# Kernel optimization log

Measured on AMD Instinct MI355X. Metric: run time of the kernel, lower is better.

Reference implementation:

```python
import jax, jax.numpy as jnp
import numpy as np


def _silu(x):
    return x * jax.nn.sigmoid(x)


def _silu_backprop(dy, x):
    s = jax.nn.sigmoid(x)
    return dy * s * (1.0 + x * (1.0 - s))


def setup_inputs() -> dict:
    key = jax.random.key(0)
    B, L, Din, Dh, Dout, C = 8, 8192, 256, 512, 256, 1024
    ks = jax.random.split(key, 9)
    w0 = jax.random.normal(ks[0], (B, Dh, Din), jnp.float32) * (Din ** -0.5)
    w1 = jax.random.normal(ks[1], (B, Dout, Dh), jnp.float32) * (Dh ** -0.5)
    w2 = jax.random.normal(ks[2], (B, Dh, Din), jnp.float32) * (Din ** -0.5)
    q = jax.random.normal(ks[3], (B, L, Din), jnp.float32)
    k = jax.random.normal(ks[4], (B, L, Din), jnp.float32)
    v = jax.random.normal(ks[5], (B, L, Dout), jnp.float32)
    # per-token learning rates (softplus-ish positive, small)
    lr0 = jax.random.uniform(ks[6], (B, L, 1), jnp.float32) * 0.01
    lr1 = jax.random.uniform(ks[7], (B, L, 1), jnp.float32) * 0.01
    lr2 = jax.random.uniform(ks[8], (B, L, 1), jnp.float32) * 0.01
    return {"w0": w0, "w1": w1, "w2": w2, "q": q, "k": k, "v": v,
            "lr0": lr0, "lr1": lr1, "lr2": lr2, "chunk_size": C}


def _apply_swiglu(w0, w1, w2, qi):
    # f(q) = w1 @ (silu(w0 @ q) * (w2 @ q)); qi: [B, C, Din] -> [B, C, Dout]
    g = jnp.einsum('bcd,bhd->bch', qi, w0)
    h = jnp.einsum('bcd,bhd->bch', qi, w2)
    return jnp.einsum('bch,boh->bco', _silu(g) * h, w1)


def reference(w0, w1, w2, q, k, v, lr0, lr1, lr2, chunk_size):
    B, L, Din = q.shape
    Dout = v.shape[-1]
    C = int(chunk_size)
    n = L // C  # seq_len assumed multiple of chunk_size
    eps = 1e-5

    # per-row norms of initial fast weights (prenorm target norms)
    w0n = jnp.linalg.norm(w0, axis=2, keepdims=True)
    w1n = jnp.linalg.norm(w1, axis=2, keepdims=True)
    w2n = jnp.linalg.norm(w2, axis=2, keepdims=True)

    def chunks(x):
        return x.reshape(B, n, C, x.shape[-1]).transpose(1, 0, 2, 3)  # [n,B,C,d]

    qc, kc, vc = chunks(q), chunks(k), chunks(v)
    l0c, l1c, l2c = chunks(lr0), chunks(lr1), chunks(lr2)

    def step(carry, xs):
        w0c, w1c, w2c, w0m, w1m, w2m = carry
        qi, ki, vi, l0, l1, l2 = xs
        # apply current fast weights to this chunk's queries
        out = _apply_swiglu(w0c, w1c, w2c, qi)
        # fast-weight SwiGLU forward on keys
        g = jnp.einsum('bcd,bhd->bch', ki, w0c)          # gate_before_act^T
        hb = jnp.einsum('bcd,bhd->bch', ki, w2c)         # hidden_before_mul^T
        sg = _silu(g)
        hidden = sg * hb                                  # [B,C,Dh]
        # backprop of dot(f(k), v) through the SwiGLU
        dh = jnp.einsum('bco,boh->bch', vi, w1c)          # dhidden^T
        dhbm = dh * sg                                    # dhidden_before_mul^T
        dg = dh * hb                                      # dgate^T
        dgba = _silu_backprop(dg, g)                      # dgate_before_act^T
        dw1 = jnp.einsum('bco,bch->boh', vi, hidden * l1)
        dw0 = jnp.einsum('bch,bcd->bhd', dgba, ki * l0)
        dw2 = jnp.einsum('bch,bcd->bhd', dhbm, ki * l2)
        # prenorm update: accumulate into main weights, renormalize rows
        w0m = w0m + dw0
        w1m = w1m + dw1
        w2m = w2m + dw2
        w0c = w0m / (jnp.linalg.norm(w0m, axis=2, keepdims=True) + eps) * w0n
        w1c = w1m / (jnp.linalg.norm(w1m, axis=2, keepdims=True) + eps) * w1n
        w2c = w2m / (jnp.linalg.norm(w2m, axis=2, keepdims=True) + eps) * w2n
        return (w0c, w1c, w2c, w0m, w1m, w2m), out

    init = (w0, w1, w2, w0, w1, w2)
    carry, outs = jax.lax.scan(
        step, init,
        (qc[:-1], kc[:-1], vc[:-1], l0c[:-1], l1c[:-1], l2c[:-1]))
    # last chunk is apply-only (shifted block-causal)
    last = _apply_swiglu(carry[0], carry[1], carry[2], qc[-1])
    out = jnp.concatenate(
        [outs.transpose(1, 0, 2, 3).reshape(B, (n - 1) * C, Dout), last], axis=1)
    return out
```

## Files before the change

### kernel.cpp

```cpp
#include <hip/hip_runtime.h>
#include <cmath>

typedef unsigned short u16;
typedef __attribute__((ext_vector_type(8))) short short8;
typedef __attribute__((ext_vector_type(4))) float f32x4;

#define DEVINL __device__ __forceinline__

constexpr int NB   = 8;
constexpr int LSEQ = 8192;
constexpr int DIN  = 256;
constexpr int DH   = 512;
constexpr int DOUT = 256;
constexpr int CHK  = 1024;
constexpr int NCHK = LSEQ / CHK;

DEVINL void split2f(float v, u16& h, u16& l) {
  unsigned u = __builtin_bit_cast(unsigned, v);
  u16 hh = (u16)(u >> 16);
  float fh = __builtin_bit_cast(float, (unsigned)hh << 16);
  float r = v - fh;
  h = hh;
  l = (u16)(__builtin_bit_cast(unsigned, r) >> 16);
}
DEVINL void split3f(float v, u16& h, u16& m, u16& l) {
  unsigned u = __builtin_bit_cast(unsigned, v);
  u16 hh = (u16)(u >> 16);
  float fh = __builtin_bit_cast(float, (unsigned)hh << 16);
  float r1 = v - fh;
  u16 mm = (u16)(__builtin_bit_cast(unsigned, r1) >> 16);
  float fm = __builtin_bit_cast(float, (unsigned)mm << 16);
  float r2 = r1 - fm;
  h = hh; m = mm;
  l = (u16)(__builtin_bit_cast(unsigned, r2) >> 16);
}

DEVINL void gl16(const u16* g, u16* l) {
  __builtin_amdgcn_global_load_lds(
      (const __attribute__((address_space(1))) unsigned int*)g,
      (__attribute__((address_space(3))) unsigned int*)l,
      16, 0, 0);
}

template<int BK> DEVINL int swz(int r) { return (BK == 64) ? (r & 7) : ((r >> 1) & 3); }

template<int BM, int BN, int BK, int NS, int DUAL, int EPI, int MERGE>
__global__ __launch_bounds__(256)
void k_gemm(const u16* A, const u16* D, const u16* B, const u16* E,
            long sLA, long sLB,
            float* __restrict__ out0, float* __restrict__ out1,
            u16* __restrict__ oh, u16* __restrict__ ol,
            int K, int ldo, long sAb, long sBb, long sOb,
            int NTX, int NTY,
            const u16* A2, const u16* B2, long sLA2, long sLB2,
            float* __restrict__ out2, int ldo2,
            long sA2b, long sB2b, long sO2b, int NTX2)
{
  constexpr int NA  = (DUAL == 1) ? 2 : 1;
  constexpr int NB_ = (DUAL == 2) ? 2 : 1;
  constexpr int NDUP = DUAL ? 2 : 1;
  constexpr int SLOTS = BK / 8;
  constexpr int RPC = 64 / SLOTS;
  constexpr int TBA = BM * BK;
  constexpr int TBB = BN * BK;
  constexpr int NTA = NA * NS, NTB = NB_ * NS;
  constexpr int CPA = BM / RPC, CPB = BN / RPC;
  constexpr int NCHUNK = NTA * CPA + NTB * CPB;
  constexpr int WM = BM / 2, WN = BN / 2, FM = WM / 16, FN = WN / 16;
  constexpr int NPROD = (NS == 2) ? 3 : 6;
  constexpr int KSTEPS = BK / 32;

  static constexpr int PSA[6] = {0, 0, 1, 0, 1, 2};
  static constexpr int PSB[6] = {0, 1, 0, 2, 1, 0};

  __shared__ alignas(16) u16 lds[(NTA * BM + NTB * BN) * BK];

  const int fid = blockIdx.x;
  const int b = fid & 7;
  int t = fid >> 3;
  int job = 0;
  if (MERGE) {
    if (t >= NTY * NTX) { job = 1; t -= NTY * NTX; }
  }
  const int ntx = (MERGE && job) ? NTX2 : NTX;
  const int my = t / ntx, nx = t % ntx;
  const int m0 = my * BM;
  const int n0 = nx * BN;

  const int tid = threadIdx.x, wid = tid >> 6, ln = tid & 63;
  const int wm = wid >> 1, wn = wid & 1;

  const u16* Ap; const u16* Dp = nullptr; const u16* Bp; const u16* Ep = nullptr;
  long eLA, eLB; int eldo; long eOb;
  if (MERGE && job) {
    Ap = A2 + (size_t)b * sA2b + (size_t)m0 * K;
    Bp = B2 + (size_t)b * sB2b + (size_t)n0 * K;
    eLA = sLA2; eLB = sLB2; eldo = ldo2; eOb = sO2b;
  } else {
    Ap = A + (size_t)b * sAb + (size_t)m0 * K;
    if (DUAL == 1) Dp = D + (size_t)b * sAb + (size_t)m0 * K;
    Bp = B + (size_t)b * sBb + (size_t)n0 * K;
    if (DUAL == 2) Ep = E + (size_t)b * sBb + (size_t)n0 * K;
    eLA = sLA; eLB = sLB; eldo = ldo; eOb = sOb;
  }

  f32x4 acc[NDUP][FM][FN];
#pragma unroll
  for (int d = 0; d < NDUP; ++d)
#pragma unroll
    for (int i = 0; i < FM; ++i)
#pragma unroll
      for (int j = 0; j < FN; ++j)
        acc[d][i][j] = (f32x4){0.f, 0.f, 0.f, 0.f};

  const int crow = ln / SLOTS;
  const int cslot = ln % SLOTS;

#pragma unroll 1
  for (int k0 = 0; k0 < K; k0 += BK) {
    for (int c = wid; c < NCHUNK; c += 4) {
      const u16* g;
      u16* ldst;
      if (c < NTA * CPA) {
        const int tile = c / CPA, rb = c % CPA;
        const int da = tile / NS, s = tile % NS;
        if (MERGE && job && da == 1) continue;
        const int r = rb * RPC + crow;
        const int kb = cslot ^ swz<BK>(r);
        const u16* base = (NA == 2 && da == 1) ? Dp : Ap;
        g = base + (size_t)s * eLA + (size_t)r * K + k0 + kb * 8;
        ldst = lds + tile * TBA + rb * (RPC * BK);
      } else {
        const int c2 = c - NTA * CPA;
        const int tile = c2 / CPB, rb = c2 % CPB;
        const int db = tile / NS, s = tile % NS;
        const int r = rb * RPC + crow;
        const int kb = cslot ^ swz<BK>(r);
        const u16* base = (NB_ == 2 && db == 1) ? Ep : Bp;
        g = base + (size_t)s * eLB + (size_t)r * K + k0 + kb * 8;
        ldst = lds + NTA * TBA + tile * TBB + rb * (RPC * BK);
      }
      gl16(g, ldst);
    }
    __syncthreads();

    const int ro = ln & 15, ko = ln >> 4;
#pragma unroll
    for (int ks = 0; ks < KSTEPS; ++ks) {
      short8 af[NA][NS][FM], bfr[NB_][NS][FN];
#pragma unroll
      for (int da = 0; da < NA; ++da) {
        if (MERGE && job && da == 1) continue;
#pragma unroll
        for (int s = 0; s < NS; ++s)
#pragma unroll
          for (int im = 0; im < FM; ++im) {
            const int row = wm * WM + im * 16 + ro;
            const int kb = ks * 4 + ko;
            const int phys = kb ^ swz<BK>(row);
            af[da][s][im] = *(const short8*)(lds + (da * NS + s) * TBA + row * BK + phys * 8);
          }
      }
#pragma unroll
      for (int db = 0; db < NB_; ++db)
#pragma unroll
        for (int s = 0; s < NS; ++s)
#pragma unroll
          for (int in = 0; in < FN; ++in) {
            const int row = wn * WN + in * 16 + ro;
            const int kb = ks * 4 + ko;
            const int phys = kb ^ swz<BK>(row);
            bfr[db][s][in] = *(const short8*)(lds + NTA * TBA + (db * NS + s) * TBB + row * BK + phys * 8);
          }
#pragma unroll
      for (int p = 0; p < NPROD; ++p) {
        const int sa = PSA[p], sb = PSB[p];
#pragma unroll
        for (int d = 0; d < NDUP; ++d) {
          if (MERGE && job && d == 1) continue;
          const int da = (DUAL == 1) ? d : 0;
          const int db = (DUAL == 2) ? d : 0;
#pragma unroll
          for (int im = 0; im < FM; ++im)
#pragma unroll
            for (int in = 0; in < FN; ++in)
              acc[d][im][in] = __builtin_amdgcn_mfma_f32_16x16x32_bf16(
                  af[da][sa][im], bfr[db][sb][in], acc[d][im][in], 0, 0, 0);
        }
      }
    }
    __syncthreads();
  }

#pragma unroll
  for (int im = 0; im < FM; ++im)
#pragma unroll
    for (int in = 0; in < FN; ++in)
#pragma unroll
      for (int r = 0; r < 4; ++r) {
        const int row = m0 + wm * WM + im * 16 + (ln >> 4) * 4 + r;
        const int col = n0 + wn * WN + in * 16 + (ln & 15);
        const size_t o = (size_t)b * eOb + (size_t)row * eldo + col;
        if (MERGE && job) {
          if (EPI == 1) out2[o] = acc[0][im][in][r];
          else          out2[o] += acc[0][im][in][r];
        } else if (EPI == 0) {
          out0[o] = acc[0][im][in][r];
        } else if (EPI == 1) {
          out0[o] = acc[0][im][in][r];
          out1[o] = acc[1][im][in][r];
        } else if (EPI == 2) {
          out0[o] += acc[0][im][in][r];
        } else if (EPI == 3) {
          out0[o] += acc[0][im][in][r];
          out1[o] += acc[1][im][in][r];
        } else {
          const float g = acc[0][im][in][r];
          const float h = acc[1][im][in][r];
          const float s = 1.f / (1.f + expf(-g));
          const float a = g * s * h;
          u16 hh, ll;
          split2f(a, hh, ll);
          oh[o] = hh;
          ol[o] = ll;
        }
      }
}

__global__ __launch_bounds__(256)
void k_bwd(const float* __restrict__ gT, const float* __restrict__ hT,
           const float* __restrict__ dT,
           const float* __restrict__ lr0, const float* __restrict__ lr1,
           const float* __restrict__ lr2,
           u16* __restrict__ gb0, u16* __restrict__ gb1, u16* __restrict__ gb2,
           u16* __restrict__ hb0, u16* __restrict__ hb1, u16* __restrict__ hb2,
           u16* __restrict__ hd0, u16* __restrict__ hd1, u16* __restrict__ hd2,
           int ch)
{
  const size_t i4 = (size_t)blockIdx.x * 256 + threadIdx.x;
  const size_t base = i4 * 4;
  const int c = (int)(base & 1023);
  const size_t bh = base >> 10;
  const int b = (int)(bh >> 9);
  const size_t li = (size_t)b * LSEQ + (size_t)ch * CHK + c;

  const float4 g4 = *(const float4*)&gT[base];
  const float4 h4 = *(const float4*)&hT[base];
  const float4 d4 = *(const float4*)&dT[base];
  const float4 L0 = *(const float4*)&lr0[li];
  const float4 L1 = *(const float4*)&lr1[li];
  const float4 L2 = *(const float4*)&lr2[li];
  const float gv[4] = {g4.x, g4.y, g4.z, g4.w};
  const float hv[4] = {h4.x, h4.y, h4.z, h4.w};
  const float dv[4] = {d4.x, d4.y, d4.z, d4.w};
  const float l0v[4] = {L0.x, L0.y, L0.z, L0.w};
  const float l1v[4] = {L1.x, L1.y, L1.z, L1.w};
  const float l2v[4] = {L2.x, L2.y, L2.z, L2.w};

  ushort4 og0, og1, og2, oh0, oh1, oh2, od0, od1, od2;
  u16* pg0 = &og0.x; u16* pg1 = &og1.x; u16* pg2 = &og2.x;
  u16* ph0 = &oh0.x; u16* ph1 = &oh1.x; u16* ph2 = &oh2.x;
  u16* pd0 = &od0.x; u16* pd1 = &od1.x; u16* pd2 = &od2.x;
#pragma unroll
  for (int t = 0; t < 4; ++t) {
    const float g = gv[t];
    const float sig = 1.f / (1.f + expf(-g));
    const float sg = g * sig;
    const float hidden = sg * hv[t];
    const float dhbm = dv[t] * sg;
    const float dgrad = dv[t] * hv[t];
    const float dgba = dgrad * sig * (1.f + g * (1.f - sig));
    split3f(dgba * l0v[t], pg0[t], pg1[t], pg2[t]);
    split3f(dhbm * l2v[t], ph0[t], ph1[t], ph2[t]);
    split3f(hidden * l1v[t], pd0[t], pd1[t], pd2[t]);
  }
  *(ushort4*)&gb0[base] = og0; *(ushort4*)&gb1[base] = og1; *(ushort4*)&gb2[base] = og2;
  *(ushort4*)&hb0[base] = oh0; *(ushort4*)&hb1[base] = oh1; *(ushort4*)&hb2[base] = oh2;
  *(ushort4*)&hd0[base] = od0; *(ushort4*)&hd1[base] = od1; *(ushort4*)&hd2[base] = od2;
}

__global__ __launch_bounds__(256)
void k_split3(const float* __restrict__ q, const float* __restrict__ k,
              const float* __restrict__ v,
              u16* __restrict__ q0, u16* __restrict__ q1,
              u16* __restrict__ k0s, u16* __restrict__ k1s, u16* __restrict__ k2s,
              u16* __restrict__ v0s, u16* __restrict__ v1s, u16* __restrict__ v2s,
              int ch)
{
  const int sec = blockIdx.y;
  const size_t base = ((size_t)blockIdx.x * 256 + threadIdx.x) * 4;
  const int b = (int)(base >> 18);
  const size_t rem = base & 0x3FFFF;
  const size_t soff = (size_t)b * (LSEQ * 256) + (size_t)ch * (CHK * 256) + rem;

  const float* src = (sec == 0) ? q : (sec == 1) ? k : v;
  const float4 x4 = *(const float4*)&src[soff];
  const float xv[4] = {x4.x, x4.y, x4.z, x4.w};

  if (sec == 0) {
    ushort4 a, bq;
    u16* pa = &a.x; u16* pb = &bq.x;
#pragma unroll
    for (int t = 0; t < 4; ++t) split2f(xv[t], pa[t], pb[t]);
    *(ushort4*)&q0[base] = a;
    *(ushort4*)&q1[base] = bq;
  } else {
    ushort4 a, bq, cq;
    u16* pa = &a.x; u16* pb = &bq.x; u16* pc = &cq.x;
#pragma unroll
    for (int t = 0; t < 4; ++t) split3f(xv[t], pa[t], pb[t], pc[t]);
    u16* d0 = (sec == 1) ? k0s : v0s;
    u16* d1 = (sec == 1) ? k1s : v1s;
    u16* d2 = (sec == 1) ? k2s : v2s;
    *(ushort4*)&d0[base] = a;
    *(ushort4*)&d1[base] = bq;
    *(ushort4*)&d2[base] = cq;
  }
}

__global__ __launch_bounds__(256)
void k_trans(const float* __restrict__ ksrc, const float* __restrict__ vsrc,
             u16* __restrict__ dk0, u16* __restrict__ dk1, u16* __restrict__ dk2,
             u16* __restrict__ dv0, u16* __restrict__ dv1, u16* __restrict__ dv2,
             int ch)
{
  __shared__ float T[64][65];
  const int b = blockIdx.z & 7;
  const int sel = blockIdx.z >> 3;
  const int ct = blockIdx.x;
  const int dt = blockIdx.y;
  const int tid = threadIdx.x;
  const float* src = sel ? vsrc : ksrc;
  u16* d0 = sel ? dv0 : dk0;
  u16* d1 = sel ? dv1 : dk1;
  u16* d2 = sel ? dv2 : dk2;
  const float* S = src + ((size_t)b * LSEQ + (size_t)ch * CHK + ct * 64) * 256 + dt * 64;

#pragma unroll
  for (int qq = 0; qq < 4; ++qq) {
    const int flat = qq * 256 + tid;
    const int r = flat >> 4;
    const int cq = (flat & 15) * 4;
    const float4 v4 = *(const float4*)&S[(size_t)r * 256 + cq];
    T[r][cq + 0] = v4.x; T[r][cq + 1] = v4.y; T[r][cq + 2] = v4.z; T[r][cq + 3] = v4.w;
  }
  __syncthreads();

  u16* D0 = d0 + (size_t)b * (256 * CHK) + (size_t)(dt * 64) * CHK + ct * 64;
  u16* D1 = d1 + (size_t)b * (256 * CHK) + (size_t)(dt * 64) * CHK + ct * 64;
  u16* D2 = d2 + (size_t)b * (256 * CHK) + (size_t)(dt * 64) * CHK + ct * 64;
#pragma unroll
  for (int qq = 0; qq < 4; ++qq) {
    const int flat = qq * 256 + tid;
    const int rr = flat >> 4;
    const int cc = (flat & 15) * 4;
    ushort4 a, bq, cq4;
    u16* pa = &a.x; u16* pb = &bq.x; u16* pc = &cq4.x;
#pragma unroll
    for (int i = 0; i < 4; ++i) split3f(T[cc + i][rr], pa[i], pb[i], pc[i]);
    const size_t o = (size_t)rr * CHK + cc;
    *(ushort4*)&D0[o] = a;
    *(ushort4*)&D1[o] = bq;
    *(ushort4*)&D2[o] = cq4;
  }
}

__global__ __launch_bounds__(256)
void k_w1t(const float* __restrict__ wm1, const float* __restrict__ scales,
           u16* __restrict__ d0, u16* __restrict__ d1, u16* __restrict__ d2)
{
  __shared__ float T[64][65];
  const int b = blockIdx.z;
  const int ot = blockIdx.x;
  const int ht = blockIdx.y;
  const int tid = threadIdx.x;
  const float* S = wm1 + (size_t)b * (256 * 512) + (size_t)(ot * 64) * 512 + ht * 64;
  const float* sc = scales + 4096 + b * 256 + ot * 64;

#pragma unroll
  for (int qq = 0; qq < 4; ++qq) {
    const int flat = qq * 256 + tid;
    const int r = flat >> 4;
    const int cq = (flat & 15) * 4;
    const float s = sc[r];
    const float4 v4 = *(const float4*)&S[(size_t)r * 512 + cq];
    T[r][cq + 0] = v4.x * s; T[r][cq + 1] = v4.y * s; T[r][cq + 2] = v4.z * s; T[r][cq + 3] = v4.w * s;
  }
  __syncthreads();

  u16* D0 = d0 + (size_t)b * (512 * 256) + (size_t)(ht * 64) * 256 + ot * 64;
  u16* D1 = d1 + (size_t)b * (512 * 256) + (size_t)(ht * 64) * 256 + ot * 64;
  u16* D2 = d2 + (size_t)b * (512 * 256) + (size_t)(ht * 64) * 256 + ot * 64;
#pragma unroll
  for (int qq = 0; qq < 4; ++qq) {
    const int flat = qq * 256 + tid;
    const int rr = flat >> 4;
    const int cc = (flat & 15) * 4;
    ushort4 a, bq, cq4;
    u16* pa = &a.x; u16* pb = &bq.x; u16* pc = &cq4.x;
#pragma unroll
    for (int i = 0; i < 4; ++i) split3f(T[cc + i][rr], pa[i], pb[i], pc[i]);
    const size_t o = (size_t)rr * 256 + cc;
    *(ushort4*)&D0[o] = a;
    *(ushort4*)&D1[o] = bq;
    *(ushort4*)&D2[o] = cq4;
  }
}

__global__ __launch_bounds__(256)
void k_wsplit(const float* __restrict__ wm0, const float* __restrict__ wm1,
              const float* __restrict__ wm2, const float* __restrict__ scales,
              u16* __restrict__ a00, u16* __restrict__ a01, u16* __restrict__ a02,
              u16* __restrict__ a10, u16* __restrict__ a11, u16* __restrict__ a12,
              u16* __restrict__ a20, u16* __restrict__ a21, u16* __restrict__ a22)
{
  const size_t e4 = ((size_t)blockIdx.x * 256 + threadIdx.x) * 4;
  const float* src; u16 *d0, *d1, *d2; float s; size_t off;
  if (e4 < 1048576) {
    off = e4; src = wm0; d0 = a00; d1 = a01; d2 = a02;
    s = scales[off >> 8];
  } else if (e4 < 2097152) {
    off = e4 - 1048576; src = wm1; d0 = a10; d1 = a11; d2 = a12;
    s = scales[4096 + (off >> 9)];
  } else {
    off = e4 - 2097152; src = wm2; d0 = a20; d1 = a21; d2 = a22;
    s = scales[6144 + (off >> 8)];
  }
  const float4 v4 = *(const float4*)&src[off];
  const float xv[4] = {v4.x * s, v4.y * s, v4.z * s, v4.w * s};
  ushort4 a, bq, cq;
  u16* pa = &a.x; u16* pb = &bq.x; u16* pc = &cq.x;
#pragma unroll
  for (int t = 0; t < 4; ++t) split3f(xv[t], pa[t], pb[t], pc[t]);
  *(ushort4*)&d0[off] = a;
  *(ushort4*)&d1[off] = bq;
  *(ushort4*)&d2[off] = cq;
}

__global__ __launch_bounds__(64)
void k_scalesplit(const float* __restrict__ wm0, const float* __restrict__ wm1,
                  const float* __restrict__ wm2, const float* __restrict__ wn,
                  float* __restrict__ scales,
                  u16* __restrict__ a00, u16* __restrict__ a01, u16* __restrict__ a02,
                  u16* __restrict__ a10, u16* __restrict__ a11, u16* __restrict__ a12,
                  u16* __restrict__ a20, u16* __restrict__ a21, u16* __restrict__ a22)
{
  const int row = blockIdx.x;
  const float* src; u16 *d0, *d1, *d2; int len; int r;
  if (row < 4096)      { r = row;        src = wm0; d0 = a00; d1 = a01; d2 = a02; len = 256; }
  else if (row < 6144) { r = row - 4096; src = wm1; d0 = a10; d1 = a11; d2 = a12; len = 512; }
  else                 { r = row - 6144; src = wm2; d0 = a20; d1 = a21; d2 = a22; len = 256; }
  const float* s = src + (size_t)r * len;
  float ss = 0.f;
  for (int i = threadIdx.x * 4; i < len; i += 256) {
    const float4 v4 = *(const float4*)&s[i];
    ss += v4.x * v4.x + v4.y * v4.y + v4.z * v4.z + v4.w * v4.w;
  }
#pragma unroll
  for (int off = 32; off > 0; off >>= 1) ss += __shfl_down(ss, off);
  ss = __shfl(ss, 0);
  const float scale = wn[row] / (sqrtf(ss) + 1e-5f);
  if (threadIdx.x == 0) scales[row] = scale;
  for (int i = threadIdx.x * 4; i < len; i += 256) {
    const float4 v4 = *(const float4*)&s[i];
    const float xv[4] = {v4.x * scale, v4.y * scale, v4.z * scale, v4.w * scale};
    ushort4 a, bq, cq;
    u16* pa = &a.x; u16* pb = &bq.x; u16* pc = &cq.x;
#pragma unroll
    for (int t = 0; t < 4; ++t) split3f(xv[t], pa[t], pb[t], pc[t]);
    const size_t o = (size_t)r * len + i;
    *(ushort4*)&d0[o] = a;
    *(ushort4*)&d1[o] = bq;
    *(ushort4*)&d2[o] = cq;
  }
}

__global__ __launch_bounds__(64)
void k_init(const float* __restrict__ w0, const float* __restrict__ w1,
            const float* __restrict__ w2,
            float* __restrict__ wm0, float* __restrict__ wm1, float* __restrict__ wm2,
            float* __restrict__ wn, float* __restrict__ scales)
{
  const int row = blockIdx.x;
  const float* src; float* dst; int len; int r;
  if (row < 4096)      { r = row;        src = w0; dst = wm0; len = 256; }
  else if (row < 6144) { r = row - 4096; src = w1; dst = wm1; len = 512; }
  else                 { r = row - 6144; src = w2; dst = wm2; len = 256; }
  const float* s = src + (size_t)r * len;
  float* d = dst + (size_t)r * len;
  float ss = 0.f;
  for (int i = threadIdx.x; i < len; i += 64) {
    const float v = s[i];
    d[i] = v;
    ss += v * v;
  }
#pragma unroll
  for (int off = 32; off > 0; off >>= 1) ss += __shfl_down(ss, off);
  if (threadIdx.x == 0) {
    wn[row] = sqrtf(ss);
    scales[row] = 1.f;
  }
}

extern "C" void kernel_launch(void* const* d_in, const int* in_sizes, int n_in,
                              void* d_out, int out_size, void* d_ws, size_t ws_size,
                              hipStream_t stream)
{
  const float* w0  = (const float*)d_in[0];
  const float* w1  = (const float*)d_in[1];
  const float* w2  = (const float*)d_in[2];
  const float* q   = (const float*)d_in[3];
  const float* k   = (const float*)d_in[4];
  const float* v   = (const float*)d_in[5];
  const float* lr0 = (const float*)d_in[6];
  const float* lr1 = (const float*)d_in[7];
  const float* lr2 = (const float*)d_in[8];
  float* out = (float*)d_out;

  float* p = (float*)d_ws;
  size_t o = 0;
  auto AF = [&](size_t n) { float* r = p + o; o += n; return r; };
  auto AH = [&](size_t n) { u16* r = (u16*)(p + o); o += n / 2; return r; };

  constexpr long WL = 1048576;
  constexpr long XL = 2097152;
  constexpr long HL = 4194304;

  float* wm0 = AF(1048576);
  float* wm1 = AF(1048576);
  float* wm2 = AF(1048576);
  float* wn = AF(10240);
  float* scales = AF(10240);
  float* gT  = AF(4194304);
  float* hT  = AF(4194304);
  float* dhT = AF(4194304);
  u16* w0s  = AH(3 * WL);
  u16* w2s  = AH(3 * WL);
  u16* w1s  = AH(3 * WL);
  u16* w1Ts = AH(3 * WL);
  u16* qs   = AH(2 * XL);
  u16* ks3  = AH(3 * XL);
  u16* vs3  = AH(3 * XL);
  u16* gbs  = AH(3 * HL);
  u16* hbs  = AH(3 * HL);
  u16* hds  = AH(3 * HL);
  u16* kTs  = ks3;
  u16* vTs  = vs3;
  u16* acts = gbs;

  k_init<<<10240, 64, 0, stream>>>(w0, w1, w2, wm0, wm1, wm2, wn, scales);
  k_wsplit<<<3072, 256, 0, stream>>>(wm0, wm1, wm2, scales,
      w0s, w0s + WL, w0s + 2 * WL, w1s, w1s + WL, w1s + 2 * WL,
      w2s, w2s + WL, w2s + 2 * WL);
  k_w1t<<<dim3(4, 8, NB), 256, 0, stream>>>(wm1, scales,
      w1Ts, w1Ts + WL, w1Ts + 2 * WL);

  for (int ch = 0; ch < NCHK; ++ch) {
    const bool last = (ch == NCHK - 1);
    k_split3<<<dim3(2048, last ? 1 : 3), 256, 0, stream>>>(q, k, v,
        qs, qs + XL, ks3, ks3 + XL, ks3 + 2 * XL, vs3, vs3 + XL, vs3 + 2 * XL, ch);

    k_gemm<128, 64, 64, 2, 2, 4, 0><<<512, 256, 0, stream>>>(
        qs, nullptr, w0s, w2s, XL, WL,
        nullptr, nullptr, acts, acts + HL,
        256, DH, 262144, 131072, (long)CHK * DH, 8, 8,
        nullptr, nullptr, 0, 0, nullptr, 0, 0, 0, 0, 0);
    k_gemm<128, 64, 64, 2, 0, 0, 0><<<256, 256, 0, stream>>>(
        acts, nullptr, w1s, nullptr, HL, WL,
        out + (size_t)ch * CHK * DOUT, nullptr, nullptr, nullptr,
        512, DOUT, (long)CHK * DH, 131072, (long)LSEQ * DOUT, 4, 8,
        nullptr, nullptr, 0, 0, nullptr, 0, 0, 0, 0, 0);

    if (last) break;

    k_gemm<64, 64, 32, 3, 1, 1, 1><<<2048, 256, 0, stream>>>(
        w0s, w2s, ks3, nullptr, WL, XL,
        gT, hT, nullptr, nullptr,
        256, CHK, 131072, 262144, (long)DH * CHK, 16, 8,
        w1Ts, vs3, WL, XL, dhT, CHK, 131072, 262144, (long)DH * CHK, 16);

    k_bwd<<<4096, 256, 0, stream>>>(gT, hT, dhT, lr0, lr1, lr2,
        gbs, gbs + HL, gbs + 2 * HL, hbs, hbs + HL, hbs + 2 * HL,
        hds, hds + HL, hds + 2 * HL, ch);

    k_trans<<<dim3(16, 4, 16), 256, 0, stream>>>(k, v,
        kTs, kTs + XL, kTs + 2 * XL, vTs, vTs + XL, vTs + 2 * XL, ch);

    k_gemm<64, 64, 32, 3, 1, 3, 1><<<512, 256, 0, stream>>>(
        gbs, hbs, kTs, nullptr, HL, XL,
        wm0, wm2, nullptr, nullptr,
        1024, DIN, (long)DH * CHK, (long)DIN * CHK, (long)DH * DIN, 4, 8,
        vTs, hds, XL, HL, wm1, DH, (long)DOUT * CHK, (long)DH * CHK,
        (long)DOUT * DH, 8);

    k_scalesplit<<<10240, 64, 0, stream>>>(wm0, wm1, wm2, wn, scales,
        w0s, w0s + WL, w0s + 2 * WL, w1s, w1s + WL, w1s + 2 * WL,
        w2s, w2s + WL, w2s + 2 * WL);
    k_w1t<<<dim3(4, 8, NB), 256, 0, stream>>>(wm1, scales,
        w1Ts, w1Ts + WL, w1Ts + 2 * WL);
  }
}
```

Baseline: 1.833 ms.

## Split-K the weight-gradient GEMM, enlarge backward tiles, reduce partials in scalesplit

The weight-gradient GEMM over the 1024-token chunk is split into four K-slices, each written as a partial into scratch buffers (gT/hT/dhT reused). The partials are summed into the main weights inside k_scalesplit, which then renormalizes and splits them. The forward-on-keys and dW GEMMs move from 64x64 to 128x128 tiles, and the fragment loads are restructured so B fragments are loaded per product pair, lowering register pressure. The intent is more data reuse per block and better parallelism for the long-K reduction. The cost is extra partial-buffer traffic and an extra read pass in scalesplit.

```diff
diff --git a/kernel.cpp b/kernel.cpp
--- a/kernel.cpp
+++ b/kernel.cpp
@@ -14,6 +14,8 @@
 constexpr int DOUT = 256;
 constexpr int CHK  = 1024;
 constexpr int NCHK = LSEQ / CHK;
+constexpr int DWSPLIT = 4;
+constexpr long PSTRIDE = 1048576;
 
 DEVINL void split2f(float v, u16& h, u16& l) {
   unsigned u = __builtin_bit_cast(unsigned, v);
@@ -44,13 +46,13 @@
 
 template<int BK> DEVINL int swz(int r) { return (BK == 64) ? (r & 7) : ((r >> 1) & 3); }
 
-template<int BM, int BN, int BK, int NS, int DUAL, int EPI, int MERGE>
+template<int BM, int BN, int BK, int NS, int DUAL, int EPI, int MERGE, int KSPLIT>
 __global__ __launch_bounds__(256)
 void k_gemm(const u16* A, const u16* D, const u16* B, const u16* E,
             long sLA, long sLB,
             float* __restrict__ out0, float* __restrict__ out1,
             u16* __restrict__ oh, u16* __restrict__ ol,
-            int K, int ldo, long sAb, long sBb, long sOb,
+            int K, int Klen, long sKp, int ldo, long sAb, long sBb, long sOb,
             int NTX, int NTY,
             const u16* A2, const u16* B2, long sLA2, long sLB2,
             float* __restrict__ out2, int ldo2,
@@ -67,11 +69,7 @@
   constexpr int CPA = BM / RPC, CPB = BN / RPC;
   constexpr int NCHUNK = NTA * CPA + NTB * CPB;
   constexpr int WM = BM / 2, WN = BN / 2, FM = WM / 16, FN = WN / 16;
-  constexpr int NPROD = (NS == 2) ? 3 : 6;
   constexpr int KSTEPS = BK / 32;
-
-  static constexpr int PSA[6] = {0, 0, 1, 0, 1, 2};
-  static constexpr int PSB[6] = {0, 1, 0, 2, 1, 0};
 
   __shared__ alignas(16) u16 lds[(NTA * BM + NTB * BN) * BK];
 
@@ -80,10 +78,12 @@
   int t = fid >> 3;
   int job = 0;
   if (MERGE) {
-    if (t >= NTY * NTX) { job = 1; t -= NTY * NTX; }
-  }
+    if (t >= NTY * NTX * KSPLIT) { job = 1; t -= NTY * NTX * KSPLIT; }
+  }
+  const int tile = t / KSPLIT;
+  const int ksid = t % KSPLIT;
   const int ntx = (MERGE && job) ? NTX2 : NTX;
-  const int my = t / ntx, nx = t % ntx;
+  const int my = tile / ntx, nx = tile % ntx;
   const int m0 = my * BM;
   const int n0 = nx * BN;
 
@@ -92,15 +92,16 @@
 
   const u16* Ap; const u16* Dp = nullptr; const u16* Bp; const u16* Ep = nullptr;
   long eLA, eLB; int eldo; long eOb;
+  const size_t kof = (size_t)ksid * Klen;
   if (MERGE && job) {
-    Ap = A2 + (size_t)b * sA2b + (size_t)m0 * K;
-    Bp = B2 + (size_t)b * sB2b + (size_t)n0 * K;
+    Ap = A2 + (size_t)b * sA2b + (size_t)m0 * K + kof;
+    Bp = B2 + (size_t)b * sB2b + (size_t)n0 * K + kof;
     eLA = sLA2; eLB = sLB2; eldo = ldo2; eOb = sO2b;
   } else {
-    Ap = A + (size_t)b * sAb + (size_t)m0 * K;
-    if (DUAL == 1) Dp = D + (size_t)b * sAb + (size_t)m0 * K;
-    Bp = B + (size_t)b * sBb + (size_t)n0 * K;
-    if (DUAL == 2) Ep = E + (size_t)b * sBb + (size_t)n0 * K;
+    Ap = A + (size_t)b * sAb + (size_t)m0 * K + kof;
+    if (DUAL == 1) Dp = D + (size_t)b * sAb + (size_t)m0 * K + kof;
+    Bp = B + (size_t)b * sBb + (size_t)n0 * K + kof;
+    if (DUAL == 2) Ep = E + (size_t)b * sBb + (size_t)n0 * K + kof;
     eLA = sLA; eLB = sLB; eldo = ldo; eOb = sOb;
   }
 
@@ -117,28 +118,28 @@
   const int cslot = ln % SLOTS;
 
 #pragma unroll 1
-  for (int k0 = 0; k0 < K; k0 += BK) {
+  for (int k0 = 0; k0 < Klen; k0 += BK) {
     for (int c = wid; c < NCHUNK; c += 4) {
       const u16* g;
       u16* ldst;
       if (c < NTA * CPA) {
-        const int tile = c / CPA, rb = c % CPA;
-        const int da = tile / NS, s = tile % NS;
+        const int tl = c / CPA, rb = c % CPA;
+        const int da = tl / NS, s = tl % NS;
         if (MERGE && job && da == 1) continue;
         const int r = rb * RPC + crow;
         const int kb = cslot ^ swz<BK>(r);
         const u16* base = (NA == 2 && da == 1) ? Dp : Ap;
         g = base + (size_t)s * eLA + (size_t)r * K + k0 + kb * 8;
-        ldst = lds + tile * TBA + rb * (RPC * BK);
+        ldst = lds + tl * TBA + rb * (RPC * BK);
       } else {
         const int c2 = c - NTA * CPA;
-        const int tile = c2 / CPB, rb = c2 % CPB;
-        const int db = tile / NS, s = tile % NS;
+        const int tl = c2 / CPB, rb = c2 % CPB;
+        const int db = tl / NS, s = tl % NS;
         const int r = rb * RPC + crow;
         const int kb = cslot ^ swz<BK>(r);
         const u16* base = (NB_ == 2 && db == 1) ? Ep : Bp;
         g = base + (size_t)s * eLB + (size_t)r * K + k0 + kb * 8;
-        ldst = lds + NTA * TBA + tile * TBB + rb * (RPC * BK);
+        ldst = lds + NTA * TBA + tl * TBB + rb * (RPC * BK);
       }
       gl16(g, ldst);
     }
@@ -147,51 +148,50 @@
     const int ro = ln & 15, ko = ln >> 4;
 #pragma unroll
     for (int ks = 0; ks < KSTEPS; ++ks) {
-      short8 af[NA][NS][FM], bfr[NB_][NS][FN];
-#pragma unroll
-      for (int da = 0; da < NA; ++da) {
-        if (MERGE && job && da == 1) continue;
-#pragma unroll
-        for (int s = 0; s < NS; ++s)
+      const int kb = ks * 4 + ko;
+#pragma unroll
+      for (int sa = 0; sa < NS; ++sa) {
+        short8 af_[NA][FM];
+#pragma unroll
+        for (int da = 0; da < NA; ++da) {
+          if (MERGE && job && da == 1) continue;
 #pragma unroll
           for (int im = 0; im < FM; ++im) {
             const int row = wm * WM + im * 16 + ro;
-            const int kb = ks * 4 + ko;
             const int phys = kb ^ swz<BK>(row);
-            af[da][s][im] = *(const short8*)(lds + (da * NS + s) * TBA + row * BK + phys * 8);
+            af_[da][im] = *(const short8*)(lds + (da * NS + sa) * TBA + row * BK + phys * 8);
           }
-      }
-#pragma unroll
-      for (int db = 0; db < NB_; ++db)
-#pragma unroll
-        for (int s = 0; s < NS; ++s)
-#pragma unroll
-          for (int in = 0; in < FN; ++in) {
-            const int row = wn * WN + in * 16 + ro;
-            const int kb = ks * 4 + ko;
-            const int phys = kb ^ swz<BK>(row);
-            bfr[db][s][in] = *(const short8*)(lds + NTA * TBA + (db * NS + s) * TBB + row * BK + phys * 8);
+        }
+#pragma unroll
+        for (int sb = 0; sb + sa < NS; ++sb) {
+          short8 bf_[NB_][FN];
+#pragma unroll
+          for (int db = 0; db < NB_; ++db)
+#pragma unroll
+            for (int in = 0; in < FN; ++in) {
+              const int row = wn * WN + in * 16 + ro;
+              const int phys = kb ^ swz<BK>(row);
+              bf_[db][in] = *(const short8*)(lds + NTA * TBA + (db * NS + sb) * TBB + row * BK + phys * 8);
+            }
+#pragma unroll
+          for (int d = 0; d < NDUP; ++d) {
+            if (MERGE && job && d == 1) continue;
+            const int da = (DUAL == 1) ? d : 0;
+            const int db = (DUAL == 2) ? d : 0;
+#pragma unroll
+            for (int im = 0; im < FM; ++im)
+#pragma unroll
+              for (int in = 0; in < FN; ++in)
+                acc[d][im][in] = __builtin_amdgcn_mfma_f32_16x16x32_bf16(
+                    af_[da][im], bf_[db][in], acc[d][im][in], 0, 0, 0);
           }
-#pragma unroll
-      for (int p = 0; p < NPROD; ++p) {
-        const int sa = PSA[p], sb = PSB[p];
-#pragma unroll
-        for (int d = 0; d < NDUP; ++d) {
-          if (MERGE && job && d == 1) continue;
-          const int da = (DUAL == 1) ? d : 0;
-          const int db = (DUAL == 2) ? d : 0;
-#pragma unroll
-          for (int im = 0; im < FM; ++im)
-#pragma unroll
-            for (int in = 0; in < FN; ++in)
-              acc[d][im][in] = __builtin_amdgcn_mfma_f32_16x16x32_bf16(
-                  af[da][sa][im], bfr[db][sb][in], acc[d][im][in], 0, 0, 0);
         }
       }
     }
     __syncthreads();
   }
 
+  const size_t kout = (size_t)ksid * sKp;
 #pragma unroll
   for (int im = 0; im < FM; ++im)
 #pragma unroll
@@ -200,7 +200,7 @@
       for (int r = 0; r < 4; ++r) {
         const int row = m0 + wm * WM + im * 16 + (ln >> 4) * 4 + r;
         const int col = n0 + wn * WN + in * 16 + (ln & 15);
-        const size_t o = (size_t)b * eOb + (size_t)row * eldo + col;
+        const size_t o = kout + (size_t)b * eOb + (size_t)row * eldo + col;
         if (MERGE && job) {
           if (EPI == 1) out2[o] = acc[0][im][in][r];
           else          out2[o] += acc[0][im][in][r];
@@ -438,36 +438,51 @@
 }
 
 __global__ __launch_bounds__(64)
-void k_scalesplit(const float* __restrict__ wm0, const float* __restrict__ wm1,
-                  const float* __restrict__ wm2, const float* __restrict__ wn,
-                  float* __restrict__ scales,
+void k_scalesplit(float* __restrict__ wm0, float* __restrict__ wm1,
+                  float* __restrict__ wm2,
+                  const float* __restrict__ p0, const float* __restrict__ p1,
+                  const float* __restrict__ p2,
+                  const float* __restrict__ wn, float* __restrict__ scales,
                   u16* __restrict__ a00, u16* __restrict__ a01, u16* __restrict__ a02,
                   u16* __restrict__ a10, u16* __restrict__ a11, u16* __restrict__ a12,
                   u16* __restrict__ a20, u16* __restrict__ a21, u16* __restrict__ a22)
 {
   const int row = blockIdx.x;
-  const float* src; u16 *d0, *d1, *d2; int len; int r;
-  if (row < 4096)      { r = row;        src = wm0; d0 = a00; d1 = a01; d2 = a02; len = 256; }
-  else if (row < 6144) { r = row - 4096; src = wm1; d0 = a10; d1 = a11; d2 = a12; len = 512; }
-  else                 { r = row - 6144; src = wm2; d0 = a20; d1 = a21; d2 = a22; len = 256; }
-  const float* s = src + (size_t)r * len;
+  float* wm; const float* pp; u16 *d0, *d1, *d2; int len; int r;
+  if (row < 4096)      { r = row;        wm = wm0; pp = p0; d0 = a00; d1 = a01; d2 = a02; len = 256; }
+  else if (row < 6144) { r = row - 4096; wm = wm1; pp = p1; d0 = a10; d1 = a11; d2 = a12; len = 512; }
+  else                 { r = row - 6144; wm = wm2; pp = p2; d0 = a20; d1 = a21; d2 = a22; len = 256; }
+  float* wrow = wm + (size_t)r * len;
+  const float* prow = pp + (size_t)r * len;
+
+  float vals[8];
+  int cnt = 0;
   float ss = 0.f;
   for (int i = threadIdx.x * 4; i < len; i += 256) {
-    const float4 v4 = *(const float4*)&s[i];
-    ss += v4.x * v4.x + v4.y * v4.y + v4.z * v4.z + v4.w * v4.w;
+    float4 w4 = *(const float4*)&wrow[i];
+    float acc4[4] = {w4.x, w4.y, w4.z, w4.w};
+#pragma unroll
+    for (int s = 0; s < DWSPLIT; ++s) {
+      const float4 q4 = *(const float4*)&prow[(size_t)s * PSTRIDE + i];
+      acc4[0] += q4.x; acc4[1] += q4.y; acc4[2] += q4.z; acc4[3] += q4.w;
+    }
+    *(float4*)&wrow[i] = make_float4(acc4[0], acc4[1], acc4[2], acc4[3]);
+#pragma unroll
+    for (int t = 0; t < 4; ++t) { vals[cnt + t] = acc4[t]; ss += acc4[t] * acc4[t]; }
+    cnt += 4;
   }
 #pragma unroll
   for (int off = 32; off > 0; off >>= 1) ss += __shfl_down(ss, off);
   ss = __shfl(ss, 0);
   const float scale = wn[row] / (sqrtf(ss) + 1e-5f);
   if (threadIdx.x == 0) scales[row] = scale;
+  cnt = 0;
   for (int i = threadIdx.x * 4; i < len; i += 256) {
-    const float4 v4 = *(const float4*)&s[i];
-    const float xv[4] = {v4.x * scale, v4.y * scale, v4.z * scale, v4.w * scale};
     ushort4 a, bq, cq;
     u16* pa = &a.x; u16* pb = &bq.x; u16* pc = &cq.x;
 #pragma unroll
-    for (int t = 0; t < 4; ++t) split3f(xv[t], pa[t], pb[t], pc[t]);
+    for (int t = 0; t < 4; ++t) split3f(vals[cnt + t] * scale, pa[t], pb[t], pc[t]);
+    cnt += 4;
     const size_t o = (size_t)r * len + i;
     *(ushort4*)&d0[o] = a;
     *(ushort4*)&d1[o] = bq;
@@ -560,24 +575,25 @@
     k_split3<<<dim3(2048, last ? 1 : 3), 256, 0, stream>>>(q, k, v,
         qs, qs + XL, ks3, ks3 + XL, ks3 + 2 * XL, vs3, vs3 + XL, vs3 + 2 * XL, ch);
 
-    k_gemm<128, 64, 64, 2, 2, 4, 0><<<512, 256, 0, stream>>>(
+    k_gemm<128, 64, 64, 2, 2, 4, 0, 1><<<512, 256, 0, stream>>>(
         qs, nullptr, w0s, w2s, XL, WL,
         nullptr, nullptr, acts, acts + HL,
-        256, DH, 262144, 131072, (long)CHK * DH, 8, 8,
+        256, 256, 0, DH, 262144, 131072, (long)CHK * DH, 8, 8,
         nullptr, nullptr, 0, 0, nullptr, 0, 0, 0, 0, 0);
-    k_gemm<128, 64, 64, 2, 0, 0, 0><<<256, 256, 0, stream>>>(
+    k_gemm<128, 64, 64, 2, 0, 0, 0, 1><<<256, 256, 0, stream>>>(
         acts, nullptr, w1s, nullptr, HL, WL,
         out + (size_t)ch * CHK * DOUT, nullptr, nullptr, nullptr,
-        512, DOUT, (long)CHK * DH, 131072, (long)LSEQ * DOUT, 4, 8,
+        512, 512, 0, DOUT, (long)CHK * DH, 131072, (long)LSEQ * DOUT,
+        4, 8,
         nullptr, nullptr, 0, 0, nullptr, 0, 0, 0, 0, 0);
 
     if (last) break;
 
-    k_gemm<64, 64, 32, 3, 1, 1, 1><<<2048, 256, 0, stream>>>(
+    k_gemm<128, 128, 32, 3, 1, 1, 1, 1><<<512, 256, 0, stream>>>(
         w0s, w2s, ks3, nullptr, WL, XL,
         gT, hT, nullptr, nullptr,
-        256, CHK, 131072, 262144, (long)DH * CHK, 16, 8,
-        w1Ts, vs3, WL, XL, dhT, CHK, 131072, 262144, (long)DH * CHK, 16);
+        256, 256, 0, CHK, 131072, 262144, (long)DH * CHK, 8, 4,
+        w1Ts, vs3, WL, XL, dhT, CHK, 131072, 262144, (long)DH * CHK, 8);
 
     k_bwd<<<4096, 256, 0, stream>>>(gT, hT, dhT, lr0, lr1, lr2,
         gbs, gbs + HL, gbs + 2 * HL, hbs, hbs + HL, hbs + 2 * HL,
@@ -586,14 +602,16 @@
     k_trans<<<dim3(16, 4, 16), 256, 0, stream>>>(k, v,
         kTs, kTs + XL, kTs + 2 * XL, vTs, vTs + XL, vTs + 2 * XL, ch);
 
-    k_gemm<64, 64, 32, 3, 1, 3, 1><<<512, 256, 0, stream>>>(
+    k_gemm<128, 128, 32, 3, 1, 1, 1, DWSPLIT><<<512, 256, 0, stream>>>(
         gbs, hbs, kTs, nullptr, HL, XL,
-        wm0, wm2, nullptr, nullptr,
-        1024, DIN, (long)DH * CHK, (long)DIN * CHK, (long)DH * DIN, 4, 8,
-        vTs, hds, XL, HL, wm1, DH, (long)DOUT * CHK, (long)DH * CHK,
-        (long)DOUT * DH, 8);
-
-    k_scalesplit<<<10240, 64, 0, stream>>>(wm0, wm1, wm2, wn, scales,
+        gT, hT, nullptr, nullptr,
+        1024, 256, PSTRIDE, DIN, (long)DH * CHK, (long)DIN * CHK,
+        (long)DH * DIN, 2, 4,
+        vTs, hds, XL, HL, dhT, DH, (long)DOUT * CHK, (long)DH * CHK,
+        (long)DOUT * DH, 4);
+
+    k_scalesplit<<<10240, 64, 0, stream>>>(wm0, wm1, wm2, gT, dhT, hT,
+        wn, scales,
         w0s, w0s + WL, w0s + 2 * WL, w1s, w1s + WL, w1s + 2 * WL,
         w2s, w2s + WL, w2s + 2 * WL);
     k_w1t<<<dim3(4, 8, NB), 256, 0, stream>>>(wm1, scales,
```

Measured after the change: 1.611 ms. 12.1% less time.
